# Kernel optimization log

Hardware: AMD Instinct MI355X
Metric: run time of the kernel (lower is better)

Reference implementation:

```python
import jax, jax.numpy as jnp
import numpy as np

N = 16384

def setup_inputs() -> dict:
    key = jax.random.key(0)
    k1, k2, k3 = jax.random.split(key, 3)
    risk_scores = jax.random.normal(k1, (N,), dtype=jnp.float32)
    survival_times = jax.random.normal(k2, (N,), dtype=jnp.float32)
    # 0/1 event indicator (1 = event observed, 0 = censored)
    events = (jax.random.uniform(k3, (N,)) < 0.5).astype(jnp.float32)
    return {"risk_scores": risk_scores, "survival_times": survival_times, "events": events}

def reference(risk_scores, survival_times, events):
    # Risk-set matrix: R[i, j] = 1 if T[j] >= T[i] (vectorized version of the
    # original O(n^2) double Python loop).
    R = (survival_times[None, :] >= survival_times[:, None]).astype(risk_scores.dtype)  # [n, n]
    exp_theta = jnp.exp(risk_scores)                # [n]
    # sum_j exp(theta_j) * R[i, j]  ->  matvec
    risk_set_sum = R @ exp_theta                    # [n]
    loss = -jnp.mean((risk_scores - jnp.log(risk_set_sum)) * events)
    return loss
```

## Files before the change

kernel.cpp:

```cpp
#include <hip/hip_runtime.h>
#include <math.h>

#define NB 1024
#define ST 1024
#define NF 16384
#define RPT 16
#define IPB 64
#define BLOCK 256

__device__ __forceinline__ int bucket_of(float t) {
    int b = (int)((t + 6.0f) * (NB / 12.0f));
    return min(max(b, 0), NB - 1);
}

__global__ __launch_bounds__(ST, 4) void surv_all(
        const float* __restrict__ theta, const float* __restrict__ T,
        const float* __restrict__ events,
        float* __restrict__ partial, int* __restrict__ ticket,
        float* __restrict__ out) {
    __shared__ float sT[NF];
    __shared__ float sE[NF];
    __shared__ int   cnt[NB];
    __shared__ float sfx[NB];
    __shared__ int   pci[ST];
    __shared__ float pce[ST];
    __shared__ int   last;

    const int tid = threadIdx.x;

    cnt[tid] = 0;
    sfx[tid] = 0.f;
    __syncthreads();

    float Ts[RPT], Es[RPT];
    #pragma unroll
    for (int r = 0; r < RPT; ++r) {
        const int j = tid + (r << 10);
        const float tv = T[j];
        const float ev = expf(theta[j]);
        Ts[r] = tv; Es[r] = ev;
        const int b = bucket_of(tv);
        atomicAdd(&cnt[b], 1);
        atomicAdd(&sfx[b], ev);
    }
    __syncthreads();

    const int   c = cnt[tid];
    const float e = sfx[tid];
    pci[tid] = c; pce[tid] = e;
    __syncthreads();
    for (int s = 1; s < ST; s <<= 1) {
        const int   a = (tid >= s)     ? pci[tid - s] : 0;
        const float f = (tid + s < ST) ? pce[tid + s] : 0.f;
        __syncthreads();
        pci[tid] += a; pce[tid] += f;
        __syncthreads();
    }
    cnt[tid] = pci[tid] - c;
    sfx[tid] = pce[tid] - e;
    __syncthreads();

    #pragma unroll
    for (int r = 0; r < RPT; ++r) {
        const int b = bucket_of(Ts[r]);
        const int pos = atomicAdd(&cnt[b], 1);
        sT[pos] = Ts[r];
        sE[pos] = Es[r];
    }
    __syncthreads();

    float term = 0.f;
    if (tid < IPB) {
        const int i = blockIdx.x * IPB + tid;
        const float Ti = T[i];
        const int b  = bucket_of(Ti);
        const int p0 = b ? cnt[b - 1] : 0;
        const int p1 = cnt[b];
        float risk = sfx[b];
        for (int p = p0; p < p1; ++p)
            risk += (sT[p] >= Ti) ? sE[p] : 0.f;
        term = (theta[i] - logf(risk)) * events[i];
        #pragma unroll
        for (int off = 32; off > 0; off >>= 1)
            term += __shfl_down(term, off, 64);
    }
    if (tid == 0) {
        partial[blockIdx.x] = term;
        __threadfence();
        last = (atomicAdd(ticket, 1) == (int)gridDim.x - 1) ? 1 : 0;
    }
    __syncthreads();
    if (last && tid < 64) {
        float v = 0.f;
        #pragma unroll
        for (int k = 0; k < 4; ++k)
            v += atomicAdd(&partial[k * 64 + tid], 0.f);
        #pragma unroll
        for (int off = 32; off > 0; off >>= 1)
            v += __shfl_down(v, off, 64);
        if (tid == 0) out[0] = -v / (float)NF;
    }
}

__global__ void surv_partial_bf(const float* __restrict__ theta, const float* __restrict__ T,
                                const float* __restrict__ events, float* __restrict__ bsum, int n) {
    __shared__ float red[BLOCK];
    const int tid = threadIdx.x;
    const int i = blockIdx.x * BLOCK + tid;
    float term = 0.f;
    if (i < n) {
        const float Ti = T[i];
        float risk = 0.f;
        for (int j = 0; j < n; ++j)
            risk += (T[j] >= Ti) ? expf(theta[j]) : 0.f;
        term = (theta[i] - logf(risk)) * events[i];
    }
    red[tid] = term;
    __syncthreads();
    for (int s = BLOCK / 2; s > 0; s >>= 1) {
        if (tid < s) red[tid] += red[tid + s];
        __syncthreads();
    }
    if (tid == 0) bsum[blockIdx.x] = red[0];
}

__global__ void surv_final(const float* __restrict__ bsum, float* __restrict__ out,
                           int nblocks, int n) {
    float v = 0.f;
    for (int b = threadIdx.x; b < nblocks; b += 64) v += bsum[b];
    for (int off = 32; off > 0; off >>= 1) v += __shfl_down(v, off, 64);
    if (threadIdx.x == 0) out[0] = -v / (float)n;
}

extern "C" void kernel_launch(void* const* d_in, const int* in_sizes, int n_in,
                              void* d_out, int out_size, void* d_ws, size_t ws_size,
                              hipStream_t stream) {
    const float* theta  = (const float*)d_in[0];
    const float* T      = (const float*)d_in[1];
    const float* events = (const float*)d_in[2];
    float* out = (float*)d_out;
    const int n = in_sizes[0];

    const size_t need = 4 + (size_t)(NF / IPB) * 4;
    const bool fast = (n == NF) && ((size_t)ws_size >= need);

    if (!fast) {
        const int nbi = (n + BLOCK - 1) / BLOCK;
        float* bsum = (float*)d_ws;
        surv_partial_bf<<<nbi, BLOCK, 0, stream>>>(theta, T, events, bsum, n);
        surv_final<<<1, 64, 0, stream>>>(bsum, out, nbi, n);
        return;
    }

    int*   ticket  = (int*)d_ws;
    float* partial = (float*)(ticket + 1);

    hipMemsetAsync(ticket, 0, 4, stream);
    surv_all<<<NF / IPB, ST, 0, stream>>>(theta, T, events, partial, ticket, out);
}
```

Before: 98.40 us.

## Replace redundant per-block bucket sort with cooperative global histogram and grid barriers

Previously every one of 256 blocks redundantly histogrammed and bucket-sorted all 16384 elements in shared memory. Now 64 blocks of 256 threads each handle one element per thread: they build a global histogram with atomics, sync through spin-wait grid barriers, each compute a prefix/suffix scan over 4096 buckets, scatter into a globally sorted buffer, and scan only their own bucket. This removes the redundant work but adds global atomics, two grid-wide spin barriers that need all 64 blocks co-resident, and a separate zeroing kernel launch.

Result: faster. 83.51 us (-15.1%).

```diff
diff --git a/kernel.cpp b/kernel.cpp
--- a/kernel.cpp
+++ b/kernel.cpp
@@ -1,11 +1,12 @@
 #include <hip/hip_runtime.h>
 #include <math.h>
 
-#define NB 1024
-#define ST 1024
 #define NF 16384
-#define RPT 16
-#define IPB 64
+#define NB 4096
+#define NBLK 64
+#define TPB 256
+#define CHUNK (NB/TPB)
+#define NZ (4 + 3*NB)
 #define BLOCK 256
 
 __device__ __forceinline__ int bucket_of(float t) {
@@ -13,92 +14,99 @@
     return min(max(b, 0), NB - 1);
 }
 
-__global__ __launch_bounds__(ST, 4) void surv_all(
+__global__ void surv_zero(int* __restrict__ w) {
+    int i = blockIdx.x * TPB + threadIdx.x;
+    if (i < NZ) w[i] = 0;
+}
+
+__global__ __launch_bounds__(TPB) void surv_pipe(
         const float* __restrict__ theta, const float* __restrict__ T,
         const float* __restrict__ events,
-        float* __restrict__ partial, int* __restrict__ ticket,
-        float* __restrict__ out) {
-    __shared__ float sT[NF];
-    __shared__ float sE[NF];
-    __shared__ int   cnt[NB];
+        int* __restrict__ bar, int* __restrict__ ticket, float* __restrict__ accum,
+        int* __restrict__ hcnt, float* __restrict__ hE, int* __restrict__ rel,
+        float2* __restrict__ sorted, float* __restrict__ out) {
+    __shared__ int   pfx[NB + 1];
     __shared__ float sfx[NB];
-    __shared__ int   pci[ST];
-    __shared__ float pce[ST];
-    __shared__ int   last;
+    __shared__ int   sc[TPB];
+    __shared__ float se[TPB];
 
     const int tid = threadIdx.x;
+    const int i   = blockIdx.x * TPB + tid;
 
-    cnt[tid] = 0;
-    sfx[tid] = 0.f;
+    const float Ti = T[i];
+    const float Ei = expf(theta[i]);
+    const int   bi = bucket_of(Ti);
+    atomicAdd(&hcnt[bi], 1);
+    atomicAdd(&hE[bi], Ei);
+
     __syncthreads();
-
-    float Ts[RPT], Es[RPT];
-    #pragma unroll
-    for (int r = 0; r < RPT; ++r) {
-        const int j = tid + (r << 10);
-        const float tv = T[j];
-        const float ev = expf(theta[j]);
-        Ts[r] = tv; Es[r] = ev;
-        const int b = bucket_of(tv);
-        atomicAdd(&cnt[b], 1);
-        atomicAdd(&sfx[b], ev);
+    if (tid == 0) {
+        __hip_atomic_fetch_add(&bar[0], 1, __ATOMIC_RELEASE, __HIP_MEMORY_SCOPE_AGENT);
+        while (__hip_atomic_load(&bar[0], __ATOMIC_ACQUIRE, __HIP_MEMORY_SCOPE_AGENT) < NBLK)
+            __builtin_amdgcn_s_sleep(8);
     }
     __syncthreads();
 
-    const int   c = cnt[tid];
-    const float e = sfx[tid];
-    pci[tid] = c; pce[tid] = e;
+    int lc[CHUNK]; float le[CHUNK];
+    const int base = tid * CHUNK;
+    int cs = 0; float es = 0.f;
+    #pragma unroll
+    for (int k = 0; k < CHUNK; ++k) {
+        lc[k] = hcnt[base + k];
+        le[k] = hE[base + k];
+        cs += lc[k]; es += le[k];
+    }
+    sc[tid] = cs; se[tid] = es;
     __syncthreads();
-    for (int s = 1; s < ST; s <<= 1) {
-        const int   a = (tid >= s)     ? pci[tid - s] : 0;
-        const float f = (tid + s < ST) ? pce[tid + s] : 0.f;
+    for (int s = 1; s < TPB; s <<= 1) {
+        int   a = (tid >= s)      ? sc[tid - s] : 0;
+        float f = (tid + s < TPB) ? se[tid + s] : 0.f;
         __syncthreads();
-        pci[tid] += a; pce[tid] += f;
+        sc[tid] += a; se[tid] += f;
         __syncthreads();
     }
-    cnt[tid] = pci[tid] - c;
-    sfx[tid] = pce[tid] - e;
-    __syncthreads();
-
-    #pragma unroll
-    for (int r = 0; r < RPT; ++r) {
-        const int b = bucket_of(Ts[r]);
-        const int pos = atomicAdd(&cnt[b], 1);
-        sT[pos] = Ts[r];
-        sE[pos] = Es[r];
+    {   int run = sc[tid] - cs;
+        #pragma unroll
+        for (int k = 0; k < CHUNK; ++k) { pfx[base + k] = run; run += lc[k]; }
+        if (tid == TPB - 1) pfx[NB] = run;
+    }
+    {   float rs = se[tid] - es;
+        #pragma unroll
+        for (int k = CHUNK - 1; k >= 0; --k) { sfx[base + k] = rs; rs += le[k]; }
     }
     __syncthreads();
 
-    float term = 0.f;
-    if (tid < IPB) {
-        const int i = blockIdx.x * IPB + tid;
-        const float Ti = T[i];
-        const int b  = bucket_of(Ti);
-        const int p0 = b ? cnt[b - 1] : 0;
-        const int p1 = cnt[b];
-        float risk = sfx[b];
-        for (int p = p0; p < p1; ++p)
-            risk += (sT[p] >= Ti) ? sE[p] : 0.f;
-        term = (theta[i] - logf(risk)) * events[i];
-        #pragma unroll
-        for (int off = 32; off > 0; off >>= 1)
-            term += __shfl_down(term, off, 64);
-    }
+    const int pos = pfx[bi] + atomicAdd(&rel[bi], 1);
+    sorted[pos] = make_float2(Ti, Ei);
+
+    __syncthreads();
     if (tid == 0) {
-        partial[blockIdx.x] = term;
-        __threadfence();
-        last = (atomicAdd(ticket, 1) == (int)gridDim.x - 1) ? 1 : 0;
+        __hip_atomic_fetch_add(&bar[1], 1, __ATOMIC_RELEASE, __HIP_MEMORY_SCOPE_AGENT);
+        while (__hip_atomic_load(&bar[1], __ATOMIC_ACQUIRE, __HIP_MEMORY_SCOPE_AGENT) < NBLK)
+            __builtin_amdgcn_s_sleep(8);
     }
     __syncthreads();
-    if (last && tid < 64) {
-        float v = 0.f;
-        #pragma unroll
-        for (int k = 0; k < 4; ++k)
-            v += atomicAdd(&partial[k * 64 + tid], 0.f);
-        #pragma unroll
-        for (int off = 32; off > 0; off >>= 1)
-            v += __shfl_down(v, off, 64);
-        if (tid == 0) out[0] = -v / (float)NF;
+
+    float risk = sfx[bi];
+    const int p1 = pfx[bi + 1];
+    for (int p = pfx[bi]; p < p1; ++p) {
+        float2 v = sorted[p];
+        risk += (v.x >= Ti) ? v.y : 0.f;
+    }
+    float term = (theta[i] - logf(risk)) * events[i];
+
+    #pragma unroll
+    for (int off = 32; off > 0; off >>= 1) term += __shfl_down(term, off, 64);
+    if ((tid & 63) == 0) se[tid >> 6] = term;
+    __syncthreads();
+    if (tid == 0) {
+        atomicAdd(accum, se[0] + se[1] + se[2] + se[3]);
+        __threadfence();
+        int t = atomicAdd(ticket, 1);
+        if (t == NBLK - 1) {
+            float tot = atomicAdd(accum, 0.f);
+            out[0] = -tot / (float)NF;
+        }
     }
 }
 
@@ -141,7 +149,7 @@
     float* out = (float*)d_out;
     const int n = in_sizes[0];
 
-    const size_t need = 4 + (size_t)(NF / IPB) * 4;
+    const size_t need = ((size_t)2 * NF + NZ) * 4;
     const bool fast = (n == NF) && ((size_t)ws_size >= need);
 
     if (!fast) {
@@ -152,9 +160,17 @@
         return;
     }
 
-    int*   ticket  = (int*)d_ws;
-    float* partial = (float*)(ticket + 1);
+    float2* sorted = (float2*)d_ws;
+    int*    meta   = (int*)d_ws + 2 * NF;
+    int*    bar    = meta;
+    int*    ticket = meta + 2;
+    float*  accum  = (float*)(meta + 3);
+    int*    hcnt   = meta + 4;
+    float*  hE     = (float*)(meta + 4 + NB);
+    int*    rel    = meta + 4 + 2 * NB;
 
-    hipMemsetAsync(ticket, 0, 4, stream);
-    surv_all<<<NF / IPB, ST, 0, stream>>>(theta, T, events, partial, ticket, out);
+    const int zb = (NZ + TPB - 1) / TPB;
+    surv_zero<<<zb, TPB, 0, stream>>>(meta);
+    surv_pipe<<<NBLK, TPB, 0, stream>>>(theta, T, events, bar, ticket, accum,
+                                        hcnt, hE, rel, sorted, out);
 }
```

## Split into global histogram kernel and bucket-range solve kernel

Applied to the files above, without the earlier changes.

Before, each of the 256 blocks rebuilt the full bucket histogram and sorted all 16384 elements into shared memory, which is heavily redundant. Now a first kernel writes per-block partial exp-sum histograms to a slab. A second kernel of 64 blocks sums the slab, builds the suffix sums, and gathers and resolves only the elements in its own bucket range. Bucket count doubles to 2048 to shorten the in-bucket scans, and the hipMemsetAsync is replaced by resetting the ticket inside the first kernel. The cost is an extra launch, a global slab round trip, and a slow fallback path if a bucket range overflows its capacity.

Measured after the change: 93.74 us. 4.7% less time.

```diff
diff --git a/kernel.cpp b/kernel.cpp
--- a/kernel.cpp
+++ b/kernel.cpp
@@ -1,11 +1,15 @@
 #include <hip/hip_runtime.h>
 #include <math.h>
 
-#define NB 1024
+#define NF 16384
+#define NB 2048
+#define HT 256
+#define HBLK (NF/HT)
 #define ST 1024
-#define NF 16384
-#define RPT 16
-#define IPB 64
+#define SBLK 64
+#define BPB (NB/SBLK)
+#define EPT (NF/ST)
+#define CAP 4096
 #define BLOCK 256
 
 __device__ __forceinline__ int bucket_of(float t) {
@@ -13,91 +17,129 @@
     return min(max(b, 0), NB - 1);
 }
 
-__global__ __launch_bounds__(ST, 4) void surv_all(
+__global__ __launch_bounds__(HT) void surv_hist(
         const float* __restrict__ theta, const float* __restrict__ T,
-        const float* __restrict__ events,
-        float* __restrict__ partial, int* __restrict__ ticket,
+        float* __restrict__ slab, int* __restrict__ ticket) {
+    __shared__ float h[NB];
+    const int tid = threadIdx.x, g = blockIdx.x;
+    #pragma unroll
+    for (int k = 0; k < NB / HT; ++k) h[tid + k * HT] = 0.f;
+    __syncthreads();
+    const int i = g * HT + tid;
+    atomicAdd(&h[bucket_of(T[i])], expf(theta[i]));
+    __syncthreads();
+    #pragma unroll
+    for (int k = 0; k < NB / HT; ++k)
+        slab[g * NB + tid + k * HT] = h[tid + k * HT];
+    if (g == 0 && tid == 0) *ticket = 0;
+}
+
+__global__ __launch_bounds__(ST) void surv_solve(
+        const float* __restrict__ theta, const float* __restrict__ T,
+        const float* __restrict__ events, const float* __restrict__ slab,
+        float* __restrict__ bsum, int* __restrict__ ticket,
         float* __restrict__ out) {
-    __shared__ float sT[NF];
-    __shared__ float sE[NF];
-    __shared__ int   cnt[NB];
     __shared__ float sfx[NB];
-    __shared__ int   pci[ST];
-    __shared__ float pce[ST];
-    __shared__ int   last;
-
-    const int tid = threadIdx.x;
-
-    cnt[tid] = 0;
-    sfx[tid] = 0.f;
-    __syncthreads();
-
-    float Ts[RPT], Es[RPT];
-    #pragma unroll
-    for (int r = 0; r < RPT; ++r) {
-        const int j = tid + (r << 10);
-        const float tv = T[j];
-        const float ev = expf(theta[j]);
-        Ts[r] = tv; Es[r] = ev;
-        const int b = bucket_of(tv);
-        atomicAdd(&cnt[b], 1);
-        atomicAdd(&sfx[b], ev);
-    }
-    __syncthreads();
-
-    const int   c = cnt[tid];
-    const float e = sfx[tid];
-    pci[tid] = c; pce[tid] = e;
+    __shared__ float se[ST];
+    __shared__ int   cntl[BPB], sbase[BPB + 1];
+    __shared__ float pT[CAP], pE[CAP];
+    __shared__ int   pJ[CAP], pB[CAP];
+    __shared__ float red[ST / 64];
+    __shared__ int   Mtot, last;
+
+    const int tid = threadIdx.x, g = blockIdx.x;
+    const int blo = g * BPB;
+
+    const int b0 = 2 * tid;
+    float e0 = 0.f, e1 = 0.f;
+    for (int s = 0; s < HBLK; ++s) {
+        const float2 v = *(const float2*)&slab[s * NB + b0];
+        e0 += v.x; e1 += v.y;
+    }
+    const float es = e0 + e1;
+    se[tid] = es;
     __syncthreads();
     for (int s = 1; s < ST; s <<= 1) {
-        const int   a = (tid >= s)     ? pci[tid - s] : 0;
-        const float f = (tid + s < ST) ? pce[tid + s] : 0.f;
-        __syncthreads();
-        pci[tid] += a; pce[tid] += f;
-        __syncthreads();
-    }
-    cnt[tid] = pci[tid] - c;
-    sfx[tid] = pce[tid] - e;
-    __syncthreads();
-
-    #pragma unroll
-    for (int r = 0; r < RPT; ++r) {
-        const int b = bucket_of(Ts[r]);
-        const int pos = atomicAdd(&cnt[b], 1);
-        sT[pos] = Ts[r];
-        sE[pos] = Es[r];
-    }
-    __syncthreads();
-
-    float term = 0.f;
-    if (tid < IPB) {
-        const int i = blockIdx.x * IPB + tid;
-        const float Ti = T[i];
-        const int b  = bucket_of(Ti);
-        const int p0 = b ? cnt[b - 1] : 0;
-        const int p1 = cnt[b];
-        float risk = sfx[b];
-        for (int p = p0; p < p1; ++p)
-            risk += (sT[p] >= Ti) ? sE[p] : 0.f;
-        term = (theta[i] - logf(risk)) * events[i];
+        const float f = (tid + s < ST) ? se[tid + s] : 0.f;
+        __syncthreads();
+        se[tid] += f;
+        __syncthreads();
+    }
+    {   const float rs = se[tid] - es;
+        sfx[b0 + 1] = rs;
+        sfx[b0]     = rs + e1;
+    }
+    if (tid < BPB) cntl[tid] = 0;
+    __syncthreads();
+
+    #pragma unroll
+    for (int k = 0; k < EPT; ++k) {
+        const int j = tid + k * ST;
+        const int b = bucket_of(T[j]) - blo;
+        if ((unsigned)b < BPB) atomicAdd(&cntl[b], 1);
+    }
+    __syncthreads();
+    if (tid == 0) {
+        int run = 0;
+        for (int b = 0; b < BPB; ++b) { sbase[b] = run; run += cntl[b]; cntl[b] = 0; }
+        sbase[BPB] = run; Mtot = run;
+    }
+    __syncthreads();
+    const int M = Mtot;
+
+    float acc = 0.f;
+    if (M <= CAP) {
         #pragma unroll
-        for (int off = 32; off > 0; off >>= 1)
-            term += __shfl_down(term, off, 64);
-    }
+        for (int k = 0; k < EPT; ++k) {
+            const int j = tid + k * ST;
+            const float Tv = T[j];
+            const int b = bucket_of(Tv) - blo;
+            if ((unsigned)b < BPB) {
+                const int pos = sbase[b] + atomicAdd(&cntl[b], 1);
+                pT[pos] = Tv; pE[pos] = expf(theta[j]); pJ[pos] = j; pB[pos] = b;
+            }
+        }
+        __syncthreads();
+        for (int e = tid; e < M; e += ST) {
+            const int b = pB[e];
+            const float Ti = pT[e];
+            float risk = sfx[blo + b];
+            const int p1 = sbase[b + 1];
+            for (int p = sbase[b]; p < p1; ++p)
+                risk += (pT[p] >= Ti) ? pE[p] : 0.f;
+            const int j = pJ[e];
+            acc += (theta[j] - logf(risk)) * events[j];
+        }
+    } else {
+        for (int j = tid; j < NF; j += ST) {
+            const float Ti = T[j];
+            const int b = bucket_of(Ti);
+            if (b < blo || b >= blo + BPB) continue;
+            float risk = sfx[b];
+            for (int j2 = 0; j2 < NF; ++j2)
+                if (bucket_of(T[j2]) == b && T[j2] >= Ti) risk += expf(theta[j2]);
+            acc += (theta[j] - logf(risk)) * events[j];
+        }
+    }
+
+    #pragma unroll
+    for (int off = 32; off > 0; off >>= 1) acc += __shfl_down(acc, off, 64);
+    if ((tid & 63) == 0) red[tid >> 6] = acc;
+    __syncthreads();
     if (tid == 0) {
-        partial[blockIdx.x] = term;
+        float bs = 0.f;
+        #pragma unroll
+        for (int w = 0; w < ST / 64; ++w) bs += red[w];
+        bsum[g] = bs;
         __threadfence();
-        last = (atomicAdd(ticket, 1) == (int)gridDim.x - 1) ? 1 : 0;
+        last = (atomicAdd(ticket, 1) == SBLK - 1) ? 1 : 0;
     }
     __syncthreads();
     if (last && tid < 64) {
-        float v = 0.f;
+        float v = atomicAdd(&bsum[tid & 63], 0.f);
+        v = (tid < SBLK) ? v : 0.f;
         #pragma unroll
-        for (int k = 0; k < 4; ++k)
-            v += atomicAdd(&partial[k * 64 + tid], 0.f);
-        #pragma unroll
-        for (int off = 32; off > 0; off >>= 1)
-            v += __shfl_down(v, off, 64);
+        for (int off = 32; off > 0; off >>= 1) v += __shfl_down(v, off, 64);
         if (tid == 0) out[0] = -v / (float)NF;
     }
 }
@@ -141,7 +183,7 @@
     float* out = (float*)d_out;
     const int n = in_sizes[0];
 
-    const size_t need = 4 + (size_t)(NF / IPB) * 4;
+    const size_t need = ((size_t)HBLK * NB + SBLK + 1) * 4;
     const bool fast = (n == NF) && ((size_t)ws_size >= need);
 
     if (!fast) {
@@ -152,9 +194,10 @@
         return;
     }
 
-    int*   ticket  = (int*)d_ws;
-    float* partial = (float*)(ticket + 1);
-
-    hipMemsetAsync(ticket, 0, 4, stream);
-    surv_all<<<NF / IPB, ST, 0, stream>>>(theta, T, events, partial, ticket, out);
-}
+    float* slab   = (float*)d_ws;
+    float* bsum   = slab + (size_t)HBLK * NB;
+    int*   ticket = (int*)(bsum + SBLK);
+
+    surv_hist<<<HBLK, HT, 0, stream>>>(theta, T, slab, ticket);
+    surv_solve<<<SBLK, ST, 0, stream>>>(theta, T, events, slab, bsum, ticket, out);
+}
```
